# Kernel tuning notes

Measured on AMD Instinct MI355X. Metric: run time of the kernel, lower is better.

The kernel has to match this reference:

```python
import jax, jax.numpy as jnp
import numpy as np

N_NODES = 100000
N_EDGES = 1600000
F_IN = 512
HEADS = 8
C1 = 8            # hidden per head in conv1
N_CLASSES = 40
NEG_SLOPE = 0.2
EPS = 1e-16


def setup_inputs() -> dict:
    key = jax.random.key(0)
    ks = jax.random.split(key, 12)
    x = jax.random.normal(ks[0], (N_NODES, F_IN), dtype=jnp.float32)
    # edges with src != dst (PyG SuperGAT removes then re-adds self-loops)
    src = jax.random.randint(ks[1], (N_EDGES,), 0, N_NODES)
    off = jax.random.randint(ks[2], (N_EDGES,), 1, N_NODES)
    dst = (src + off) % N_NODES
    edge_index = jnp.stack([src, dst]).astype(jnp.int64)
    def glorot(k, shape):
        fan = shape[0] + shape[-1]
        return jax.random.uniform(k, shape, jnp.float32, -1.0, 1.0) * np.sqrt(6.0 / fan)
    W1 = glorot(ks[3], (F_IN, HEADS * C1))
    att_l1 = glorot(ks[4], (HEADS, C1))
    att_r1 = glorot(ks[5], (HEADS, C1))
    b1 = jnp.zeros((HEADS * C1,), jnp.float32)
    W2 = glorot(ks[6], (HEADS * C1, HEADS * N_CLASSES))
    att_l2 = glorot(ks[7], (HEADS, N_CLASSES))
    att_r2 = glorot(ks[8], (HEADS, N_CLASSES))
    b2 = jnp.zeros((N_CLASSES,), jnp.float32)
    return {"x": x, "edge_index": edge_index, "W1": W1, "att_l1": att_l1,
            "att_r1": att_r1, "b1": b1, "W2": W2, "att_l2": att_l2,
            "att_r2": att_r2, "b2": b2}


def supergat_conv(x, edge_index, W, att_l, att_r, bias, concat):
    """SuperGATConv with attention_type='MX', eval mode (no dropout)."""
    N = x.shape[0]
    H, C = att_l.shape
    xw = (x @ W).reshape(N, H, C)
    loops = jnp.arange(N)
    src = jnp.concatenate([edge_index[0], loops])  # j (source)
    dst = jnp.concatenate([edge_index[1], loops])  # i (target)
    x_j = xw[src]                                   # [E,H,C]
    x_i = xw[dst]                                   # [E,H,C]
    # MX attention: GO score gated by sigmoid of DP logits
    logits = jnp.einsum('ehc,ehc->eh', x_i, x_j)
    alpha = jnp.einsum('ehc,hc->eh', x_j, att_l) + jnp.einsum('ehc,hc->eh', x_i, att_r)
    alpha = alpha * jax.nn.sigmoid(logits)
    alpha = jax.nn.leaky_relu(alpha, NEG_SLOPE)
    # segment softmax over incoming edges of each destination node
    amax = jax.ops.segment_max(alpha, dst, num_segments=N)
    e = jnp.exp(alpha - amax[dst])
    denom = jax.ops.segment_sum(e, dst, num_segments=N)
    a = e / (denom[dst] + EPS)
    out = jax.ops.segment_sum(x_j * a[..., None], dst, num_segments=N)  # [N,H,C]
    out = out.reshape(N, H * C) if concat else out.mean(axis=1)
    return out + bias


def reference(x, edge_index, W1, att_l1, att_r1, b1, W2, att_l2, att_r2, b2):
    # eval mode: F.dropout(p=0.6) is identity, att_loss is 0
    h = jax.nn.elu(supergat_conv(x, edge_index, W1, att_l1, att_r1, b1, concat=True))
    out = supergat_conv(h, edge_index, W2, att_l2, att_r2, b2, concat=False)
    att_loss = jnp.float32(0.0)
    return jax.nn.log_softmax(out, axis=-1), att_loss
```

## Files before the change

### kernel.cpp

```cpp
#include <hip/hip_runtime.h>
#include <cstdint>

#define N_NODES 100000
#define N_EDGES 1600000
#define SCAN_NB 196

typedef short bf16x8 __attribute__((ext_vector_type(8)));
typedef float f32x4 __attribute__((ext_vector_type(4)));
typedef float f32x2 __attribute__((ext_vector_type(2)));

__device__ __forceinline__ uint16_t f2bf(float f) {
    uint32_t b = __float_as_uint(f);
    return (uint16_t)((b + 0x7fffu + ((b >> 16) & 1u)) >> 16);
}
__device__ __forceinline__ float bfval(uint16_t u) {
    return __uint_as_float(((uint32_t)u) << 16);
}
__device__ __forceinline__ float blo(uint32_t u) { return __uint_as_float(u << 16); }
__device__ __forceinline__ float bhi(uint32_t u) { return __uint_as_float(u & 0xffff0000u); }

__device__ __forceinline__ float fast_rcp(float x) { return __builtin_amdgcn_rcpf(x); }
__device__ __forceinline__ float dpp_xadd1(float x) {
    int s = __builtin_amdgcn_update_dpp(0, __float_as_int(x), 0xB1, 0xF, 0xF, true);
    return x + __int_as_float(s);
}
__device__ __forceinline__ float dpp_xadd2(float x) {
    int s = __builtin_amdgcn_update_dpp(0, __float_as_int(x), 0x4E, 0xF, 0xF, true);
    return x + __int_as_float(s);
}

__global__ __launch_bounds__(512) void prep_hist_k(const float* __restrict__ W1,
        const float* __restrict__ W2, const float* __restrict__ attl,
        const float* __restrict__ attr,
        uint16_t* __restrict__ w1hi, uint16_t* __restrict__ w1lo,
        float* __restrict__ wl2, float* __restrict__ wr2,
        uint16_t* __restrict__ w2T,
        const int* __restrict__ dst, int* __restrict__ deg) {
    int b = blockIdx.x, tid = threadIdx.x;
    if (b >= 10) {
        int e = (b - 10) * 512 + tid;
        if (e < N_EDGES) atomicAdd(&deg[dst[e]], 1);
        return;
    }
    if (b < 8) {
        int gid = b * 512 + tid;
        int c = gid & 63, kg = gid >> 6;
        uint32_t dh[4], dl[4];
        #pragma unroll
        for (int t = 0; t < 4; ++t) {
            float v0 = W1[(kg * 8 + 2 * t) * 64 + c];
            float v1 = W1[(kg * 8 + 2 * t + 1) * 64 + c];
            uint16_t h0 = f2bf(v0), h1 = f2bf(v1);
            uint16_t l0 = f2bf(v0 - bfval(h0)), l1 = f2bf(v1 - bfval(h1));
            dh[t] = h0 | ((uint32_t)h1 << 16);
            dl[t] = l0 | ((uint32_t)l1 << 16);
        }
        *(uint4*)(w1hi + (long)c * 512 + kg * 8) = make_uint4(dh[0], dh[1], dh[2], dh[3]);
        *(uint4*)(w1lo + (long)c * 512 + kg * 8) = make_uint4(dl[0], dl[1], dl[2], dl[3]);
    } else if (b == 8) {
        int h = tid >> 6, k = tid & 63;
        float sl = 0.f, sr = 0.f;
        #pragma unroll 8
        for (int c = 0; c < 40; ++c) {
            float w = W2[k * 320 + h * 40 + c];
            sl += w * attl[h * 40 + c];
            sr += w * attr[h * 40 + c];
        }
        wl2[tid] = sl; wr2[tid] = sr;
    } else {
        int c = tid;
        if (c < 320) {
            for (int kg = 0; kg < 8; ++kg) {
                uint32_t d[4];
                #pragma unroll
                for (int t = 0; t < 4; ++t) {
                    float v0 = W2[(kg * 8 + 2 * t) * 320 + c];
                    float v1 = W2[(kg * 8 + 2 * t + 1) * 320 + c];
                    d[t] = f2bf(v0) | ((uint32_t)f2bf(v1) << 16);
                }
                *(uint4*)(w2T + (long)c * 64 + kg * 8) = make_uint4(d[0], d[1], d[2], d[3]);
            }
        }
    }
}

__global__ __launch_bounds__(512) void scan_a(const int* __restrict__ deg,
        int* __restrict__ offs, int* __restrict__ btot) {
    __shared__ int sh[512];
    int t = threadIdx.x;
    int g = blockIdx.x * 512 + t;
    int v = (g < N_NODES) ? deg[g] : 0;
    sh[t] = v;
    __syncthreads();
    #pragma unroll
    for (int o = 1; o < 512; o <<= 1) {
        int add = (t >= o) ? sh[t - o] : 0;
        __syncthreads();
        sh[t] += add;
        __syncthreads();
    }
    if (g < N_NODES) offs[g] = sh[t] - v;
    if (t == 511) btot[blockIdx.x] = sh[511];
}

__global__ __launch_bounds__(256) void scan_b(int* __restrict__ btot) {
    __shared__ int sh[256];
    int t = threadIdx.x;
    int v = (t < SCAN_NB) ? btot[t] : 0;
    sh[t] = v;
    __syncthreads();
    #pragma unroll
    for (int o = 1; o < 256; o <<= 1) {
        int add = (t >= o) ? sh[t - o] : 0;
        __syncthreads();
        sh[t] += add;
        __syncthreads();
    }
    if (t < SCAN_NB) btot[t] = sh[t] - v;
}

__global__ __launch_bounds__(512) void gemm1_scatter(const float* __restrict__ x,
        const uint16_t* __restrict__ w1hi, const uint16_t* __restrict__ w1lo,
        float* __restrict__ xw1, uint16_t* __restrict__ xw1b,
        const int* __restrict__ src, const int* __restrict__ dst,
        int* __restrict__ offs, const int* __restrict__ btot,
        int* __restrict__ csr8) {
    __shared__ __align__(16) char Ah[128 * 144];
    __shared__ __align__(16) char Al[128 * 144];
    __shared__ __align__(16) char Bh[64 * 144];
    __shared__ __align__(16) char Bl[64 * 144];
    int tid = threadIdx.x;
    if (blockIdx.x >= 782) {
        int base = (blockIdx.x - 782) * 1024 + tid;
        #pragma unroll
        for (int r = 0; r < 2; ++r) {
            int e = base + r * 512;
            if (e < N_EDGES) {
                int d = dst[e];
                int old = atomicAdd(&offs[d], 1);
                csr8[btot[d >> 9] + old] = src[e] << 3;
            }
        }
        return;
    }
    int l = tid & 63, w = tid >> 6;
    long base = (long)blockIdx.x * 128;
    f32x4 acc[4];
    #pragma unroll
    for (int ct = 0; ct < 4; ++ct)
        #pragma unroll
        for (int j = 0; j < 4; ++j) acc[ct][j] = 0.f;

    for (int kb = 0; kb < 512; kb += 64) {
        __syncthreads();
        #pragma unroll
        for (int it = 0; it < 2; ++it) {
            int idx = tid + it * 512;
            int row = idx >> 3, kc = idx & 7;
            long r = base + row; if (r >= N_NODES) r = N_NODES - 1;
            const float4* p = (const float4*)(x + r * 512 + kb + kc * 8);
            float4 f0 = p[0], f1 = p[1];
            float v[8] = {f0.x, f0.y, f0.z, f0.w, f1.x, f1.y, f1.z, f1.w};
            uint32_t dh[4], dl[4];
            #pragma unroll
            for (int t = 0; t < 4; ++t) {
                uint16_t h0 = f2bf(v[2 * t]),     h1 = f2bf(v[2 * t + 1]);
                uint16_t l0 = f2bf(v[2 * t] - bfval(h0));
                uint16_t l1 = f2bf(v[2 * t + 1] - bfval(h1));
                dh[t] = h0 | ((uint32_t)h1 << 16);
                dl[t] = l0 | ((uint32_t)l1 << 16);
            }
            *(uint4*)(Ah + row * 144 + kc * 16) = make_uint4(dh[0], dh[1], dh[2], dh[3]);
            *(uint4*)(Al + row * 144 + kc * 16) = make_uint4(dl[0], dl[1], dl[2], dl[3]);
        }
        {
            int c = tid >> 3, kc = tid & 7;
            *(uint4*)(Bh + c * 144 + kc * 16) =
                *(const uint4*)(w1hi + (long)c * 512 + kb + kc * 8);
            *(uint4*)(Bl + c * 144 + kc * 16) =
                *(const uint4*)(w1lo + (long)c * 512 + kb + kc * 8);
        }
        __syncthreads();
        #pragma unroll
        for (int kk = 0; kk < 2; ++kk) {
            int aoff = (w * 16 + (l & 15)) * 144 + kk * 64 + (l >> 4) * 16;
            bf16x8 ah = *(const bf16x8*)(Ah + aoff);
            bf16x8 alo = *(const bf16x8*)(Al + aoff);
            #pragma unroll
            for (int ct = 0; ct < 4; ++ct) {
                int boff = (ct * 16 + (l & 15)) * 144 + kk * 64 + (l >> 4) * 16;
                bf16x8 bh = *(const bf16x8*)(Bh + boff);
                bf16x8 bl = *(const bf16x8*)(Bl + boff);
                acc[ct] = __builtin_amdgcn_mfma_f32_16x16x32_bf16(ah, bh, acc[ct], 0, 0, 0);
                acc[ct] = __builtin_amdgcn_mfma_f32_16x16x32_bf16(alo, bh, acc[ct], 0, 0, 0);
                acc[ct] = __builtin_amdgcn_mfma_f32_16x16x32_bf16(ah, bl, acc[ct], 0, 0, 0);
            }
        }
    }
    int nrow = w * 16 + (l >> 4) * 4;
    #pragma unroll
    for (int ct = 0; ct < 4; ++ct)
        #pragma unroll
        for (int j = 0; j < 4; ++j) {
            long node = base + nrow + j;
            if (node < N_NODES) {
                int col = ct * 16 + (l & 15);
                xw1[node * 64 + col] = acc[ct][j];
                xw1b[node * 64 + col] = f2bf(acc[ct][j]);
            }
        }
}

__global__ __launch_bounds__(512) void gemm2_mfma(const float* __restrict__ h,
        const uint16_t* __restrict__ w2T, uint16_t* __restrict__ xw2) {
    __shared__ __align__(16) char Bsm[320 * 144];
    int tid = threadIdx.x;
    int l = tid & 63, w = tid >> 6;
    long base = (long)blockIdx.x * 128;
    #pragma unroll
    for (int it = 0; it < 5; ++it) {
        int idx = tid + it * 512;
        int c = idx >> 3, kc = idx & 7;
        *(uint4*)(Bsm + c * 144 + kc * 16) = *(const uint4*)(w2T + (long)c * 64 + kc * 8);
    }
    long n0 = base + w * 16 + (l & 15);
    long nld = n0 < N_NODES ? n0 : N_NODES - 1;
    bf16x8 ah[2], alo[2];
    #pragma unroll
    for (int kk = 0; kk < 2; ++kk) {
        const float4* p = (const float4*)(h + nld * 64 + kk * 32 + (l >> 4) * 8);
        float4 f0 = p[0], f1 = p[1];
        float v[8] = {f0.x, f0.y, f0.z, f0.w, f1.x, f1.y, f1.z, f1.w};
        bf16x8 hv, lv;
        #pragma unroll
        for (int t = 0; t < 8; ++t) {
            uint16_t hh = f2bf(v[t]);
            hv[t] = (short)hh;
            lv[t] = (short)f2bf(v[t] - bfval(hh));
        }
        ah[kk] = hv; alo[kk] = lv;
    }
    __syncthreads();
    f32x4 acc[20];
    #pragma unroll
    for (int ct = 0; ct < 20; ++ct)
        #pragma unroll
        for (int j = 0; j < 4; ++j) acc[ct][j] = 0.f;
    #pragma unroll
    for (int ct = 0; ct < 20; ++ct) {
        #pragma unroll
        for (int kk = 0; kk < 2; ++kk) {
            bf16x8 b = *(const bf16x8*)(Bsm + (ct * 16 + (l & 15)) * 144 + kk * 64 + (l >> 4) * 16);
            acc[ct] = __builtin_amdgcn_mfma_f32_16x16x32_bf16(b, ah[kk], acc[ct], 0, 0, 0);
            acc[ct] = __builtin_amdgcn_mfma_f32_16x16x32_bf16(b, alo[kk], acc[ct], 0, 0, 0);
        }
    }
    if (n0 < N_NODES) {
        #pragma unroll
        for (int ct = 0; ct < 20; ++ct) {
            uint32_t d0 = f2bf(acc[ct][0]) | ((uint32_t)f2bf(acc[ct][1]) << 16);
            uint32_t d1 = f2bf(acc[ct][2]) | ((uint32_t)f2bf(acc[ct][3]) << 16);
            int cb = ct * 16 + (l >> 4) * 4;
            *(uint32_t*)(xw2 + n0 * 320 + cb) = d0;
            *(uint32_t*)(xw2 + n0 * 320 + cb + 2) = d1;
        }
    }
}

__global__ __launch_bounds__(256) void conv1_node(const float* __restrict__ xw,
        const uint16_t* __restrict__ xwb,
        const int* __restrict__ offs, const int* __restrict__ deg,
        const int* __restrict__ btot,
        const int* __restrict__ csr8, const float* __restrict__ att_l,
        const float* __restrict__ att_r, const float* __restrict__ b1,
        const float* __restrict__ wl2, const float* __restrict__ wr2,
        float* __restrict__ hout, float* __restrict__ al, float* __restrict__ ar) {
    int wid = (blockIdx.x * blockDim.x + threadIdx.x) >> 6;
    if (wid >= N_NODES) return;
    int i = wid;
    int lane = threadIdx.x & 63;
    int g = lane >> 3, h = lane & 7;
    const float4* rowi = (const float4*)(xw + (long)i * 64 + h * 8);
    float4 xi0 = rowi[0], xi1 = rowi[1];
    f32x2 xip[4] = {{xi0.x, xi0.y}, {xi0.z, xi0.w}, {xi1.x, xi1.y}, {xi1.z, xi1.w}};
    const float4* alp4 = (const float4*)(att_l + h * 8);
    float4 t0 = alp4[0], t1 = alp4[1];
    f32x2 atlp[4] = {{t0.x, t0.y}, {t0.z, t0.w}, {t1.x, t1.y}, {t1.z, t1.w}};
    const float4* arp4 = (const float4*)(att_r + h * 8);
    float4 u0 = arp4[0], u1 = arp4[1];
    f32x2 atrp[4] = {{u0.x, u0.y}, {u0.z, u0.w}, {u1.x, u1.y}, {u1.z, u1.w}};
    f32x2 prp = xip[0] * atrp[0];
    prp += xip[1] * atrp[1];
    prp += xip[2] * atrp[2];
    prp += xip[3] * atrp[3];
    float pr = prp.x + prp.y;
    f32x2 accp[4] = {{0.f,0.f},{0.f,0.f},{0.f,0.f},{0.f,0.f}};
    float den = 0.f;

#define C1_EDGE(XJP) do { \
    f32x2 qdp = xip[0] * (XJP)[0]; \
    qdp += xip[1] * (XJP)[1]; \
    qdp += xip[2] * (XJP)[2]; \
    qdp += xip[3] * (XJP)[3]; \
    f32x2 qlp = (XJP)[0] * atlp[0]; \
    qlp += (XJP)[1] * atlp[1]; \
    qlp += (XJP)[2] * atlp[2]; \
    qlp += (XJP)[3] * atlp[3]; \
    float qd = qdp.x + qdp.y, ql = qlp.x + qlp.y; \
    float a = (ql + pr) * fast_rcp(1.0f + __expf(-qd)); \
    a = fmaxf(a, 0.2f * a); \
    float e = __expf(a); \
    den += e; \
    f32x2 ev = {e, e}; \
    accp[0] += ev * (XJP)[0]; \
    accp[1] += ev * (XJP)[1]; \
    accp[2] += ev * (XJP)[2]; \
    accp[3] += ev * (XJP)[3]; \
} while (0)

    if (g == 0) C1_EDGE(xip);
    int dg = deg[i];
    int off = btot[i >> 9] + offs[i] - dg;
    int k = g;
    for (; k + 8 < dg; k += 16) {
        int j0 = csr8[off + k], j1 = csr8[off + k + 8];
        uint4 q0 = *(const uint4*)(xwb + (long)j0 * 8 + h * 8);
        uint4 q1 = *(const uint4*)(xwb + (long)j1 * 8 + h * 8);
        f32x2 ap[4] = {{blo(q0.x), bhi(q0.x)}, {blo(q0.y), bhi(q0.y)},
                       {blo(q0.z), bhi(q0.z)}, {blo(q0.w), bhi(q0.w)}};
        f32x2 bp[4] = {{blo(q1.x), bhi(q1.x)}, {blo(q1.y), bhi(q1.y)},
                       {blo(q1.z), bhi(q1.z)}, {blo(q1.w), bhi(q1.w)}};
        C1_EDGE(ap);
        C1_EDGE(bp);
    }
    if (k < dg) {
        int j0 = csr8[off + k];
        uint4 q0 = *(const uint4*)(xwb + (long)j0 * 8 + h * 8);
        f32x2 ap[4] = {{blo(q0.x), bhi(q0.x)}, {blo(q0.y), bhi(q0.y)},
                       {blo(q0.z), bhi(q0.z)}, {blo(q0.w), bhi(q0.w)}};
        C1_EDGE(ap);
    }
#undef C1_EDGE

    float acc[8] = {accp[0].x, accp[0].y, accp[1].x, accp[1].y,
                    accp[2].x, accp[2].y, accp[3].x, accp[3].y};
    #pragma unroll
    for (int o = 8; o <= 32; o <<= 1) {
        #pragma unroll
        for (int t = 0; t < 8; ++t) acc[t] += __shfl_xor(acc[t], o);
        den += __shfl_xor(den, o);
    }
    float inv = fast_rcp(den + 1e-16f);
    const float4* bp4 = (const float4*)(b1 + h * 8);
    float4 c0 = bp4[0], c1 = bp4[1];
    float bias[8] = {c0.x, c0.y, c0.z, c0.w, c1.x, c1.y, c1.z, c1.w};
    float ov[8];
    #pragma unroll
    for (int t = 0; t < 8; ++t) {
        float v = acc[t] * inv + bias[t];
        ov[t] = v > 0.f ? v : __expf(v) - 1.0f;
    }
    if (g == 0) {
        float4* po = (float4*)(hout + (long)i * 64 + h * 8);
        po[0] = make_float4(ov[0], ov[1], ov[2], ov[3]);
        po[1] = make_float4(ov[4], ov[5], ov[6], ov[7]);
    }
    {
        const float4* wlp = (const float4*)(wl2 + g * 64 + h * 8);
        float4 w0 = wlp[0], w1 = wlp[1];
        const float4* wrp = (const float4*)(wr2 + g * 64 + h * 8);
        float4 r0 = wrp[0], r1 = wrp[1];
        float sl = ov[0]*w0.x + ov[1]*w0.y + ov[2]*w0.z + ov[3]*w0.w
                 + ov[4]*w1.x + ov[5]*w1.y + ov[6]*w1.z + ov[7]*w1.w;
        float sr = ov[0]*r0.x + ov[1]*r0.y + ov[2]*r0.z + ov[3]*r0.w
                 + ov[4]*r1.x + ov[5]*r1.y + ov[6]*r1.z + ov[7]*r1.w;
        #pragma unroll
        for (int o = 1; o <= 4; o <<= 1) {
            sl += __shfl_xor(sl, o);
            sr += __shfl_xor(sr, o);
        }
        if (h == 0) {
            al[i * 8 + g] = sl;
            ar[i * 8 + g] = sr;
        }
    }
}

__device__ __forceinline__ int fidx(const int* __restrict__ csr8, int pos, int valid) {
    int p = pos < N_EDGES ? pos : N_EDGES - 1;
    int j = csr8[p];
    return valid ? j : 0;
}

__global__ __launch_bounds__(256) void conv2_node(const uint16_t* __restrict__ xw,
        const int* __restrict__ offs, const int* __restrict__ deg,
        const int* __restrict__ btot,
        const int* __restrict__ csr8, const float* __restrict__ al,
        const float* __restrict__ ar, const float* __restrict__ b2,
        float* __restrict__ out) {
    if (blockIdx.x == 0 && threadIdx.x == 0) out[(long)N_NODES * 40] = 0.0f;
    int wid = (blockIdx.x * blockDim.x + threadIdx.x) >> 6;
    if (wid >= N_NODES) return;
    int i = wid;
    int lane = threadIdx.x & 63;
    int half = lane >> 5, l = lane & 31;
    int h = l >> 2, q = l & 3;
    const uint32_t* xwd = (const uint32_t*)xw;
    unsigned lq4 = 20u * (unsigned)h + 4u * (unsigned)q;
    unsigned lq1 = 20u * (unsigned)h + 16u + (unsigned)q;

    f32x2 xip[5];
    {
        const uint32_t* rowi = xwd + (unsigned)i * 160u;
        uint4 qi = *(const uint4*)(rowi + lq4);
        uint32_t ti = rowi[lq1];
        xip[0] = (f32x2){blo(qi.x), bhi(qi.x)};
        xip[1] = (f32x2){blo(qi.y), bhi(qi.y)};
        xip[2] = (f32x2){blo(qi.z), bhi(qi.z)};
        xip[3] = (f32x2){blo(qi.w), bhi(qi.w)};
        xip[4] = (f32x2){blo(ti),   bhi(ti)};
    }
    float ari = ar[i * 8 + h];
    f32x2 accp[5] = {{0.f,0.f},{0.f,0.f},{0.f,0.f},{0.f,0.f},{0.f,0.f}};
    float den = 0.f;

#define C2_CORE(ALJ, XJP) do { \
    f32x2 pdp = xip[0] * (XJP)[0]; \
    pdp += xip[1] * (XJP)[1]; \
    pdp += xip[2] * (XJP)[2]; \
    pdp += xip[3] * (XJP)[3]; \
    pdp += xip[4] * (XJP)[4]; \
    float pd = pdp.x + pdp.y; \
    pd = dpp_xadd1(pd); \
    pd = dpp_xadd2(pd); \
    float a = ((ALJ) + ari) * fast_rcp(1.0f + __expf(-pd)); \
    a = fmaxf(a, 0.2f * a); \
    float e = __expf(a); \
    den += e; \
    f32x2 ev = {e, e}; \
    accp[0] += ev * (XJP)[0]; \
    accp[1] += ev * (XJP)[1]; \
    accp[2] += ev * (XJP)[2]; \
    accp[3] += ev * (XJP)[3]; \
    accp[4] += ev * (XJP)[4]; \
} while (0)

#define C2_UNPACK(DST, U) do { \
    _Pragma("unroll") \
    for (int t = 0; t < 5; ++t) (DST)[t] = (f32x2){blo((U)[t]), bhi((U)[t])}; \
} while (0)

#define C2_FETCH(J, BUF, ALV) do { \
    const uint32_t* _r = xwd + (unsigned)(J) * 20u; \
    uint4 _q = *(const uint4*)(_r + lq4); \
    (BUF)[0] = _q.x; (BUF)[1] = _q.y; (BUF)[2] = _q.z; (BUF)[3] = _q.w; \
    (BUF)[4] = _r[lq1]; \
    (ALV) = al[(J) + h]; \
} while (0)

    if (half == 0) C2_CORE(al[i * 8 + h], xip);
    int dg = deg[i];
    int off = btot[i >> 9] + offs[i] - dg;

    int k = half;
    int v0 = (k < dg), v1 = (k + 2 < dg);
    int j0 = fidx(csr8, off + k, v0);
    int j1 = fidx(csr8, off + k + 2, v1);
    uint32_t cA[5], cB[5], dA[5], dB[5];
    float alA, alB, alC, alD;
    C2_FETCH(j0, cA, alA);
    C2_FETCH(j1, cB, alB);
    while (v0) {
        int k4 = k + 4;
        int w0 = (k4 < dg), w1 = (k4 + 2 < dg);
        int m0 = fidx(csr8, off + k4, w0);
        int m1 = fidx(csr8, off + k4 + 2, w1);
        C2_FETCH(m0, dA, alC);
        C2_FETCH(m1, dB, alD);
        { f32x2 xj[5]; C2_UNPACK(xj, cA); C2_CORE(alA, xj); }
        if (v1) { f32x2 xj[5]; C2_UNPACK(xj, cB); C2_CORE(alB, xj); }
        if (!w0) break;
        int k8 = k + 8;
        v0 = (k8 < dg); v1 = (k8 + 2 < dg);
        int p0 = fidx(csr8, off + k8, v0);
        int p1 = fidx(csr8, off + k8 + 2, v1);
        C2_FETCH(p0, cA, alA);
        C2_FETCH(p1, cB, alB);
        { f32x2 xj[5]; C2_UNPACK(xj, dA); C2_CORE(alC, xj); }
        if (w1) { f32x2 xj[5]; C2_UNPACK(xj, dB); C2_CORE(alD, xj); }
        k = k8;
    }
#undef C2_CORE
#undef C2_UNPACK
#undef C2_FETCH

    float acc[10] = {accp[0].x, accp[0].y, accp[1].x, accp[1].y, accp[2].x,
                     accp[2].y, accp[3].x, accp[3].y, accp[4].x, accp[4].y};
    #pragma unroll
    for (int t = 0; t < 10; ++t) acc[t] += __shfl_xor(acc[t], 32);
    den += __shfl_xor(den, 32);
    float inv = 0.125f * fast_rcp(den + 1e-16f);
    #pragma unroll
    for (int t = 0; t < 10; ++t) acc[t] *= inv;
    #pragma unroll
    for (int o = 4; o <= 16; o <<= 1) {
        #pragma unroll
        for (int t = 0; t < 10; ++t) acc[t] += __shfl_xor(acc[t], o);
    }
    #pragma unroll
    for (int t = 0; t < 8; ++t) acc[t] += b2[8 * q + t];
    acc[8] += b2[32 + 2 * q];
    acc[9] += b2[33 + 2 * q];
    float mx = acc[0];
    #pragma unroll
    for (int t = 1; t < 10; ++t) mx = fmaxf(mx, acc[t]);
    mx = fmaxf(mx, __shfl_xor(mx, 1));
    mx = fmaxf(mx, __shfl_xor(mx, 2));
    float s = 0.f;
    #pragma unroll
    for (int t = 0; t < 10; ++t) s += __expf(acc[t] - mx);
    s += __shfl_xor(s, 1);
    s += __shfl_xor(s, 2);
    float lse = mx + __logf(s);
    if (lane < 4) {
        float4* po = (float4*)(out + (long)i * 40 + 8 * q);
        po[0] = make_float4(acc[0] - lse, acc[1] - lse, acc[2] - lse, acc[3] - lse);
        po[1] = make_float4(acc[4] - lse, acc[5] - lse, acc[6] - lse, acc[7] - lse);
        float2* pt = (float2*)(out + (long)i * 40 + 32 + 2 * q);
        *pt = make_float2(acc[8] - lse, acc[9] - lse);
    }
}

extern "C" void kernel_launch(void* const* d_in, const int* in_sizes, int n_in,
                              void* d_out, int out_size, void* d_ws, size_t ws_size,
                              hipStream_t stream) {
    const float* x      = (const float*)d_in[0];
    const int*   ei     = (const int*)d_in[1];
    const float* W1     = (const float*)d_in[2];
    const float* att_l1 = (const float*)d_in[3];
    const float* att_r1 = (const float*)d_in[4];
    const float* b1     = (const float*)d_in[5];
    const float* W2     = (const float*)d_in[6];
    const float* att_l2 = (const float*)d_in[7];
    const float* att_r2 = (const float*)d_in[8];
    const float* b2     = (const float*)d_in[9];
    const int* src = ei;
    const int* dst = ei + N_EDGES;
    float* out = (float*)d_out;

    char* ws = (char*)d_ws;
    float*    xw1    = (float*)(ws + 0);
    float*    hbuf   = (float*)(ws + 25600000);
    uint16_t* xw2b   = (uint16_t*)(ws + 51200000);
    uint16_t* xw1b   = (uint16_t*)(ws + 51200000);
    float*    al     = (float*)(ws + 115200000);
    float*    ar     = (float*)(ws + 118400000);
    int*      deg    = (int*)(ws + 121600000);
    int*      offs   = (int*)(ws + 122000000);
    int*      btot   = (int*)(ws + 122800000);
    int*      csr8   = (int*)(ws + 122801024);
    uint16_t* w1hi   = (uint16_t*)(ws + 129201024);
    uint16_t* w1lo   = (uint16_t*)(ws + 129266560);
    uint16_t* w2T    = (uint16_t*)(ws + 129332096);
    float*    wl2    = (float*)(ws + 129373056);
    float*    wr2    = (float*)(ws + 129375104);

    hipMemsetAsync(deg, 0, (size_t)N_NODES * 4, stream);

    prep_hist_k<<<3135, 512, 0, stream>>>(W1, W2, att_l2, att_r2,
                                          w1hi, w1lo, wl2, wr2, w2T, dst, deg);

    scan_a<<<SCAN_NB, 512, 0, stream>>>(deg, offs, btot);
    scan_b<<<1, 256, 0, stream>>>(btot);

    gemm1_scatter<<<2345, 512, 0, stream>>>(x, w1hi, w1lo, xw1, xw1b,
                                            src, dst, offs, btot, csr8);

    conv1_node<<<25000, 256, 0, stream>>>(xw1, xw1b, offs, deg, btot, csr8,
                                          att_l1, att_r1, b1, wl2, wr2,
                                          hbuf, al, ar);

    gemm2_mfma<<<782, 512, 0, stream>>>(hbuf, w2T, xw2b);
    conv2_node<<<25000, 256, 0, stream>>>(xw2b, offs, deg, btot, csr8, al, ar, b2, out);
}
```

Baseline: 471.1 us.

## Use packed bf16 conversion, fuse scan kernels, drop fp32 xw1 output

Replaces software bf16 rounding with the hardware v_cvt_pk_bf16_f32 instruction in all conversion sites. Merges the two scan kernels into one using a last-block-done atomic counter, which is zeroed by extending the existing memset. Removes the fp32 xw1 store from gemm1 and has conv1 read the self row from the bf16 copy, cutting write traffic at some cost in precision for the x_i terms.

Result: slower. 487.1 us (+3.4%).

```diff
diff --git a/kernel.cpp b/kernel.cpp
--- a/kernel.cpp
+++ b/kernel.cpp
@@ -18,6 +18,11 @@
 }
 __device__ __forceinline__ float blo(uint32_t u) { return __uint_as_float(u << 16); }
 __device__ __forceinline__ float bhi(uint32_t u) { return __uint_as_float(u & 0xffff0000u); }
+__device__ __forceinline__ uint32_t cvtpk(float a, float b) {
+    uint32_t r;
+    asm("v_cvt_pk_bf16_f32 %0, %1, %2" : "=v"(r) : "v"(a), "v"(b));
+    return r;
+}
 
 __device__ __forceinline__ float fast_rcp(float x) { return __builtin_amdgcn_rcpf(x); }
 __device__ __forceinline__ float dpp_xadd1(float x) {
@@ -50,10 +55,8 @@
         for (int t = 0; t < 4; ++t) {
             float v0 = W1[(kg * 8 + 2 * t) * 64 + c];
             float v1 = W1[(kg * 8 + 2 * t + 1) * 64 + c];
-            uint16_t h0 = f2bf(v0), h1 = f2bf(v1);
-            uint16_t l0 = f2bf(v0 - bfval(h0)), l1 = f2bf(v1 - bfval(h1));
-            dh[t] = h0 | ((uint32_t)h1 << 16);
-            dl[t] = l0 | ((uint32_t)l1 << 16);
+            dh[t] = cvtpk(v0, v1);
+            dl[t] = cvtpk(v0 - blo(dh[t]), v1 - bhi(dh[t]));
         }
         *(uint4*)(w1hi + (long)c * 512 + kg * 8) = make_uint4(dh[0], dh[1], dh[2], dh[3]);
         *(uint4*)(w1lo + (long)c * 512 + kg * 8) = make_uint4(dl[0], dl[1], dl[2], dl[3]);
@@ -76,7 +79,7 @@
                 for (int t = 0; t < 4; ++t) {
                     float v0 = W2[(kg * 8 + 2 * t) * 320 + c];
                     float v1 = W2[(kg * 8 + 2 * t + 1) * 320 + c];
-                    d[t] = f2bf(v0) | ((uint32_t)f2bf(v1) << 16);
+                    d[t] = cvtpk(v0, v1);
                 }
                 *(uint4*)(w2T + (long)c * 64 + kg * 8) = make_uint4(d[0], d[1], d[2], d[3]);
             }
@@ -84,13 +87,15 @@
     }
 }
 
-__global__ __launch_bounds__(512) void scan_a(const int* __restrict__ deg,
-        int* __restrict__ offs, int* __restrict__ btot) {
+__global__ __launch_bounds__(512) void scan_ab(const int* __restrict__ deg,
+        int* __restrict__ offs, int* __restrict__ btot, int* __restrict__ done) {
     __shared__ int sh[512];
+    __shared__ int lastFlag;
     int t = threadIdx.x;
     int g = blockIdx.x * 512 + t;
     int v = (g < N_NODES) ? deg[g] : 0;
     sh[t] = v;
+    if (t == 0) lastFlag = 0;
     __syncthreads();
     #pragma unroll
     for (int o = 1; o < 512; o <<= 1) {
@@ -100,28 +105,35 @@
         __syncthreads();
     }
     if (g < N_NODES) offs[g] = sh[t] - v;
-    if (t == 511) btot[blockIdx.x] = sh[511];
-}
-
-__global__ __launch_bounds__(256) void scan_b(int* __restrict__ btot) {
-    __shared__ int sh[256];
-    int t = threadIdx.x;
-    int v = (t < SCAN_NB) ? btot[t] : 0;
-    sh[t] = v;
+    if (t == 511)
+        __hip_atomic_store(&btot[blockIdx.x], sh[511], __ATOMIC_RELEASE,
+                           __HIP_MEMORY_SCOPE_AGENT);
     __syncthreads();
-    #pragma unroll
-    for (int o = 1; o < 256; o <<= 1) {
-        int add = (t >= o) ? sh[t - o] : 0;
+    if (t == 0) {
+        int old = __hip_atomic_fetch_add(done, 1, __ATOMIC_ACQ_REL,
+                                         __HIP_MEMORY_SCOPE_AGENT);
+        if (old == SCAN_NB - 1) lastFlag = 1;
+    }
+    __syncthreads();
+    if (lastFlag) {
+        int v2 = (t < SCAN_NB) ? __hip_atomic_load(&btot[t], __ATOMIC_ACQUIRE,
+                                                   __HIP_MEMORY_SCOPE_AGENT) : 0;
+        if (t < 256) sh[t] = v2;
         __syncthreads();
-        sh[t] += add;
-        __syncthreads();
-    }
-    if (t < SCAN_NB) btot[t] = sh[t] - v;
+        #pragma unroll
+        for (int o = 1; o < 256; o <<= 1) {
+            int add = (t >= o && t < 256) ? sh[t - o] : 0;
+            __syncthreads();
+            if (t < 256) sh[t] += add;
+            __syncthreads();
+        }
+        if (t < SCAN_NB) btot[t] = sh[t] - v2;
+    }
 }
 
 __global__ __launch_bounds__(512) void gemm1_scatter(const float* __restrict__ x,
         const uint16_t* __restrict__ w1hi, const uint16_t* __restrict__ w1lo,
-        float* __restrict__ xw1, uint16_t* __restrict__ xw1b,
+        uint16_t* __restrict__ xw1b,
         const int* __restrict__ src, const int* __restrict__ dst,
         int* __restrict__ offs, const int* __restrict__ btot,
         int* __restrict__ csr8) {
@@ -164,11 +176,8 @@
             uint32_t dh[4], dl[4];
             #pragma unroll
             for (int t = 0; t < 4; ++t) {
-                uint16_t h0 = f2bf(v[2 * t]),     h1 = f2bf(v[2 * t + 1]);
-                uint16_t l0 = f2bf(v[2 * t] - bfval(h0));
-                uint16_t l1 = f2bf(v[2 * t + 1] - bfval(h1));
-                dh[t] = h0 | ((uint32_t)h1 << 16);
-                dl[t] = l0 | ((uint32_t)l1 << 16);
+                dh[t] = cvtpk(v[2 * t], v[2 * t + 1]);
+                dl[t] = cvtpk(v[2 * t] - blo(dh[t]), v[2 * t + 1] - bhi(dh[t]));
             }
             *(uint4*)(Ah + row * 144 + kc * 16) = make_uint4(dh[0], dh[1], dh[2], dh[3]);
             *(uint4*)(Al + row * 144 + kc * 16) = make_uint4(dl[0], dl[1], dl[2], dl[3]);
@@ -205,7 +214,6 @@
             long node = base + nrow + j;
             if (node < N_NODES) {
                 int col = ct * 16 + (l & 15);
-                xw1[node * 64 + col] = acc[ct][j];
                 xw1b[node * 64 + col] = f2bf(acc[ct][j]);
             }
         }
@@ -231,14 +239,16 @@
         const float4* p = (const float4*)(h + nld * 64 + kk * 32 + (l >> 4) * 8);
         float4 f0 = p[0], f1 = p[1];
         float v[8] = {f0.x, f0.y, f0.z, f0.w, f1.x, f1.y, f1.z, f1.w};
-        bf16x8 hv, lv;
-        #pragma unroll
-        for (int t = 0; t < 8; ++t) {
-            uint16_t hh = f2bf(v[t]);
-            hv[t] = (short)hh;
-            lv[t] = (short)f2bf(v[t] - bfval(hh));
-        }
-        ah[kk] = hv; alo[kk] = lv;
+        uint32_t ph[4], pl[4];
+        #pragma unroll
+        for (int t = 0; t < 4; ++t) {
+            ph[t] = cvtpk(v[2 * t], v[2 * t + 1]);
+            pl[t] = cvtpk(v[2 * t] - blo(ph[t]), v[2 * t + 1] - bhi(ph[t]));
+        }
+        uint4 uh = make_uint4(ph[0], ph[1], ph[2], ph[3]);
+        uint4 ul = make_uint4(pl[0], pl[1], pl[2], pl[3]);
+        ah[kk]  = *(bf16x8*)&uh;
+        alo[kk] = *(bf16x8*)&ul;
     }
     __syncthreads();
     f32x4 acc[20];
@@ -258,8 +268,8 @@
     if (n0 < N_NODES) {
         #pragma unroll
         for (int ct = 0; ct < 20; ++ct) {
-            uint32_t d0 = f2bf(acc[ct][0]) | ((uint32_t)f2bf(acc[ct][1]) << 16);
-            uint32_t d1 = f2bf(acc[ct][2]) | ((uint32_t)f2bf(acc[ct][3]) << 16);
+            uint32_t d0 = cvtpk(acc[ct][0], acc[ct][1]);
+            uint32_t d1 = cvtpk(acc[ct][2], acc[ct][3]);
             int cb = ct * 16 + (l >> 4) * 4;
             *(uint32_t*)(xw2 + n0 * 320 + cb) = d0;
             *(uint32_t*)(xw2 + n0 * 320 + cb + 2) = d1;
@@ -267,8 +277,7 @@
     }
 }
 
-__global__ __launch_bounds__(256) void conv1_node(const float* __restrict__ xw,
-        const uint16_t* __restrict__ xwb,
+__global__ __launch_bounds__(256) void conv1_node(const uint16_t* __restrict__ xwb,
         const int* __restrict__ offs, const int* __restrict__ deg,
         const int* __restrict__ btot,
         const int* __restrict__ csr8, const float* __restrict__ att_l,
@@ -280,9 +289,9 @@
     int i = wid;
     int lane = threadIdx.x & 63;
     int g = lane >> 3, h = lane & 7;
-    const float4* rowi = (const float4*)(xw + (long)i * 64 + h * 8);
-    float4 xi0 = rowi[0], xi1 = rowi[1];
-    f32x2 xip[4] = {{xi0.x, xi0.y}, {xi0.z, xi0.w}, {xi1.x, xi1.y}, {xi1.z, xi1.w}};
+    uint4 qi = *(const uint4*)(xwb + (long)i * 64 + h * 8);
+    f32x2 xip[4] = {{blo(qi.x), bhi(qi.x)}, {blo(qi.y), bhi(qi.y)},
+                    {blo(qi.z), bhi(qi.z)}, {blo(qi.w), bhi(qi.w)}};
     const float4* alp4 = (const float4*)(att_l + h * 8);
     float4 t0 = alp4[0], t1 = alp4[1];
     f32x2 atlp[4] = {{t0.x, t0.y}, {t0.z, t0.w}, {t1.x, t1.y}, {t1.z, t1.w}};
@@ -549,7 +558,6 @@
     float* out = (float*)d_out;
 
     char* ws = (char*)d_ws;
-    float*    xw1    = (float*)(ws + 0);
     float*    hbuf   = (float*)(ws + 25600000);
     uint16_t* xw2b   = (uint16_t*)(ws + 51200000);
     uint16_t* xw1b   = (uint16_t*)(ws + 51200000);
@@ -557,6 +565,7 @@
     float*    ar     = (float*)(ws + 118400000);
     int*      deg    = (int*)(ws + 121600000);
     int*      offs   = (int*)(ws + 122000000);
+    int*      done   = (int*)(ws + 122400000);
     int*      btot   = (int*)(ws + 122800000);
     int*      csr8   = (int*)(ws + 122801024);
     uint16_t* w1hi   = (uint16_t*)(ws + 129201024);
@@ -565,18 +574,17 @@
     float*    wl2    = (float*)(ws + 129373056);
     float*    wr2    = (float*)(ws + 129375104);
 
-    hipMemsetAsync(deg, 0, (size_t)N_NODES * 4, stream);
+    hipMemsetAsync(deg, 0, 800004, stream);
 
     prep_hist_k<<<3135, 512, 0, stream>>>(W1, W2, att_l2, att_r2,
                                           w1hi, w1lo, wl2, wr2, w2T, dst, deg);
 
-    scan_a<<<SCAN_NB, 512, 0, stream>>>(deg, offs, btot);
-    scan_b<<<1, 256, 0, stream>>>(btot);
-
-    gemm1_scatter<<<2345, 512, 0, stream>>>(x, w1hi, w1lo, xw1, xw1b,
+    scan_ab<<<SCAN_NB, 512, 0, stream>>>(deg, offs, btot, done);
+
+    gemm1_scatter<<<2345, 512, 0, stream>>>(x, w1hi, w1lo, xw1b,
                                             src, dst, offs, btot, csr8);
 
-    conv1_node<<<25000, 256, 0, stream>>>(xw1, xw1b, offs, deg, btot, csr8,
+    conv1_node<<<25000, 256, 0, stream>>>(xw1b, offs, deg, btot, csr8,
                                           att_l1, att_r1, b1, wl2, wr2,
                                           hbuf, al, ar);
 
```
